# Optimization experiments

Hardware: AMD Instinct MI355X
Metric: run time of the kernel (lower is better)

Reference implementation:

```python
import jax, jax.numpy as jnp
import numpy as np

SIGMA = 1.0
MU = 1.0
STRIKE = 3.0
N_STEPS = 256
BATCH = 131072


def setup_inputs() -> dict:
    key = jax.random.key(0)
    ks = jax.random.split(key, 4)

    def lin(k, o, i):
        # equinox Linear-style uniform init in [-1/sqrt(i), 1/sqrt(i)]
        lim = 1.0 / np.sqrt(i)
        return jax.random.uniform(k, (o, i), jnp.float32, -lim, lim)

    return {
        "noise": jax.random.normal(ks[0], (N_STEPS, BATCH), jnp.float32),
        "ts": jnp.linspace(0.0, 1.0, N_STEPS + 1, dtype=jnp.float32),
        "w": jnp.float32(0.9),  # E[max(S1 - K, 0)] Monte-Carlo constant
        "W1": lin(ks[1], 32, 2), "b1": jnp.zeros((32,), jnp.float32),
        "W2": lin(ks[2], 32, 32), "b2": jnp.zeros((32,), jnp.float32),
        "W3": lin(ks[3], 1, 32), "b3": jnp.zeros((1,), jnp.float32),
    }


def reference(noise, ts, w, W1, b1, W2, b2, W3, b3):
    # Holding strategy MLP: in=[t, s] (2) -> 32 -> 32 -> 1, silu/silu/sigmoid
    def holding(t, s):  # s: [B] -> h: [B]
        x = jnp.stack([jnp.broadcast_to(t, s.shape), s], axis=-1)  # [B,2]
        a = jax.nn.silu(x @ W1.T + b1)
        a = jax.nn.silu(a @ W2.T + b2)
        return jax.nn.sigmoid(a @ W3.T + b3)[:, 0]

    def drift(t, y):  # y: [B,2] -> [B,2]
        s = y[:, 0]
        h = holding(t, s)
        return jnp.stack([MU * s, MU * s * h], axis=-1)

    def diffusion(t, y):  # scalar Brownian noise: diffusion vector [B,2]
        s = y[:, 0]
        h = holding(t, s)
        return jnp.stack([SIGMA * s, SIGMA * s * h], axis=-1)

    dts = jnp.diff(ts)                      # [N]
    dWs = noise * jnp.sqrt(dts)[:, None]    # [N,B] Brownian increments

    def step(y, xs):
        t, dt, dW = xs                      # dW: [B]
        f = drift(t, y)
        g = diffusion(t, y)
        # Milstein correction: directional derivative (Dg . g) via jvp
        _, dg = jax.jvp(lambda yy: diffusion(t, yy), (y,), (g,))
        y1 = (y + f * dt + g * dW[:, None]
              + 0.5 * dg * (dW * dW - dt)[:, None])  # Ito Milstein
        return y1, None

    B = noise.shape[1]
    y0 = jnp.broadcast_to(jnp.array([1.0, 0.0], jnp.float32), (B, 2))
    yT, _ = jax.lax.scan(step, y0, (ts[:-1], dts, dWs))

    s1 = yT[:, 0]
    hedging_pnl = yT[:, 1]
    z = jnp.maximum(0.0, s1 - STRIKE)
    return (z - hedging_pnl - w) ** 2  # [B] per-path loss
```

## Files before the change

### kernel.cpp

```cpp
#include <hip/hip_runtime.h>
#include <hip/hip_fp16.h>
#include <math.h>

#define BATCH 131072
#define NSTEPS 256
#define LGN 7
#define NPTS 128
#define ZSPAN 12.0f
#define ZLO 6.0f
#define ZSCALE (NPTS / ZSPAN)
#define DZ (ZSPAN / NPTS)
#define MU_C 0.72134752044448170367f
#define SD_C 1.4426950408889634f

using f32x2 = __attribute__((ext_vector_type(2))) float;

__device__ __forceinline__ float fast_exp(float x) {
    return __builtin_amdgcn_exp2f(x * 1.44269504088896340736f);
}
__device__ __forceinline__ float fast_rcp(float x) {
    return __builtin_amdgcn_rcpf(x);
}
__device__ __forceinline__ float sigmoidf_fast(float x) {
    return fast_rcp(1.0f + fast_exp(-x));
}

#define REP32(M) M(0) M(1) M(2) M(3) M(4) M(5) M(6) M(7) \
                 M(8) M(9) M(10) M(11) M(12) M(13) M(14) M(15) \
                 M(16) M(17) M(18) M(19) M(20) M(21) M(22) M(23) \
                 M(24) M(25) M(26) M(27) M(28) M(29) M(30) M(31)

#define REP16(M) M(0) M(1) M(2) M(3) M(4) M(5) M(6) M(7) \
                 M(8) M(9) M(10) M(11) M(12) M(13) M(14) M(15)

#define MLP_BODY(W1r, B1, W2r, B2, W3r, b3v, t, s, sd, H, HACC) \
    { \
        const float __t = (t), __s = (s), __sd = (sd); \
        f32x2 acc2 = {(b3v), 0.0f}; \
        REP32(MLP_L1) \
        REP32(MLP_ROW) \
        H = sigmoidf_fast(acc2.x); \
        HACC = acc2.y; \
    }

#define MLP_L1(j) f32x2 at##j; { \
    const float2 wv = W1r[j]; \
    const float z  = fmaf(wv.x, __t, fmaf(wv.y, __s, B1[j])); \
    const float zd = wv.y * __sd; \
    const float sg = sigmoidf_fast(z); \
    const float da = sg * (1.0f + z * (1.0f - sg)); \
    at##j = (f32x2){z * sg, da * zd}; }

#define MLP_ROW(j) { \
    const float4 q0 = W2r[(j) * 8 + 0]; \
    const float4 q1 = W2r[(j) * 8 + 1]; \
    const float4 q2 = W2r[(j) * 8 + 2]; \
    const float4 q3 = W2r[(j) * 8 + 3]; \
    const float4 q4 = W2r[(j) * 8 + 4]; \
    const float4 q5 = W2r[(j) * 8 + 5]; \
    const float4 q6 = W2r[(j) * 8 + 6]; \
    const float4 q7 = W2r[(j) * 8 + 7]; \
    f32x2 zza = {B2[j], 0.0f}; \
    f32x2 zzb = {0.0f, 0.0f}; \
    zza += (f32x2){q0.x, q0.x} * at0;  zzb += (f32x2){q0.y, q0.y} * at1; \
    zza += (f32x2){q0.z, q0.z} * at2;  zzb += (f32x2){q0.w, q0.w} * at3; \
    zza += (f32x2){q1.x, q1.x} * at4;  zzb += (f32x2){q1.y, q1.y} * at5; \
    zza += (f32x2){q1.z, q1.z} * at6;  zzb += (f32x2){q1.w, q1.w} * at7; \
    zza += (f32x2){q2.x, q2.x} * at8;  zzb += (f32x2){q2.y, q2.y} * at9; \
    zza += (f32x2){q2.z, q2.z} * at10; zzb += (f32x2){q2.w, q2.w} * at11; \
    zza += (f32x2){q3.x, q3.x} * at12; zzb += (f32x2){q3.y, q3.y} * at13; \
    zza += (f32x2){q3.z, q3.z} * at14; zzb += (f32x2){q3.w, q3.w} * at15; \
    zza += (f32x2){q4.x, q4.x} * at16; zzb += (f32x2){q4.y, q4.y} * at17; \
    zza += (f32x2){q4.z, q4.z} * at18; zzb += (f32x2){q4.w, q4.w} * at19; \
    zza += (f32x2){q5.x, q5.x} * at20; zzb += (f32x2){q5.y, q5.y} * at21; \
    zza += (f32x2){q5.z, q5.z} * at22; zzb += (f32x2){q5.w, q5.w} * at23; \
    zza += (f32x2){q6.x, q6.x} * at24; zzb += (f32x2){q6.y, q6.y} * at25; \
    zza += (f32x2){q6.z, q6.z} * at26; zzb += (f32x2){q6.w, q6.w} * at27; \
    zza += (f32x2){q7.x, q7.x} * at28; zzb += (f32x2){q7.y, q7.y} * at29; \
    zza += (f32x2){q7.z, q7.z} * at30; zzb += (f32x2){q7.w, q7.w} * at31; \
    const f32x2 zzt = zza + zzb; \
    const float zv  = zzt.x; \
    const float sg  = sigmoidf_fast(zv); \
    const float da  = sg * (1.0f + zv * (1.0f - sg)); \
    const float w3  = W3r[j]; \
    acc2 += (f32x2){w3, w3} * (f32x2){zv * sg, da * zzt.y}; \
}

__global__ __launch_bounds__(256) void table_eval_kernel(
    const float* __restrict__ ts,
    const float* __restrict__ W1, const float* __restrict__ b1,
    const float* __restrict__ W2, const float* __restrict__ b2,
    const float* __restrict__ W3, const float* __restrict__ b3,
    unsigned int* __restrict__ W)
{
    __shared__ __align__(16) float sW1[64];
    __shared__ float sb1[32];
    __shared__ __align__(16) float sW2[1024];
    __shared__ float sb2[32];
    __shared__ float sW3[32];
    __shared__ float sb3[1];

    const int tid = threadIdx.x;
    for (int i = tid; i < 1024; i += 256) sW2[i] = W2[i];
    if (tid < 64) sW1[tid] = W1[tid];
    if (tid < 32) { sb1[tid] = b1[tid]; sb2[tid] = b2[tid]; sW3[tid] = W3[tid]; }
    if (tid == 0) sb3[0] = b3[0];
    __syncthreads();

    const float2* W1r = (const float2*)sW1;
    const float*  B1  = sb1;
    const float4* W2r = (const float4*)sW2;
    const float*  B2  = sb2;
    const float*  W3r = sW3;
    const float   b3v = sb3[0];

    const int gid = blockIdx.x * 256 + tid;
    const int st = gid >> LGN;
    const int k  = gid & (NPTS - 1);

    const float t  = ts[st];
    const float mu = MU_C * t;
    const float sd = SD_C * __builtin_sqrtf(t) + 1e-4f;
    const float zz = fmaf((float)k, DZ, -ZLO);
    const float s  = __builtin_amdgcn_exp2f(fmaf(zz, sd, mu));

    float h, hacc;
    MLP_BODY(W1r, B1, W2r, B2, W3r, b3v, t, s, 1.0f, h, hacc)

    const float q = h * (1.0f - h) * hacc * s;
    __half2 p = __floats2half2_rn(h, q);
    const unsigned int pv = *(unsigned int*)&p;

    W[2 * gid] = pv;
    if (k > 0)         W[2 * gid - 1] = pv;
    if (k == NPTS - 1) W[2 * gid + 1] = pv;
}

__global__ __launch_bounds__(256, 1) void path_kernel(
    const float* __restrict__ noise,
    const float* __restrict__ ts,
    const float* __restrict__ wq,
    const uint2* __restrict__ T2,
    float* __restrict__ out)
{
    __shared__ float4 sdt4[NSTEPS];
    __shared__ float  scr[NSTEPS];
    const int tid = threadIdx.x;
    if (tid < NSTEPS) {
        const float t0  = ts[tid];
        const float dtv = ts[tid + 1] - t0;
        const float sdv = SD_C * __builtin_sqrtf(t0) + 1e-4f;
        const float wp  = fast_rcp(sdv) * ZSCALE;
        const float cp  = ZLO * ZSCALE - MU_C * t0 * wp;
        sdt4[tid] = make_float4(dtv, __builtin_sqrtf(dtv), cp, wp);
        scr[tid]  = 0.69314718056f * fast_rcp(wp);
    }
    __syncthreads();

    const int gid = blockIdx.x * 256 + tid;
    const float* np_ = noise + gid;
    const float umax = (float)NPTS - 1.001f;

    float s   = 1.0f;
    float pnl = 0.0f;

    #define NL0(k) float nA##k = np_[(size_t)(k) * BATCH]; \
                   float nB##k = np_[(size_t)(16 + k) * BATCH];
    REP16(NL0)
    #undef NL0

    #define CHK(k, G, NPv, BASE) \
        const float4 dq##G##k = sdt4[(BASE) + k]; \
        const float dW##G##k  = NPv##k * dq##G##k.y; \
        const float mil##G##k = 0.5f * fmaf(dW##G##k, dW##G##k, -dq##G##k.x); \
        const float Af##G##k  = dq##G##k.x + dW##G##k + mil##G##k; \
        const float sv##G##k  = s; \
        s = fmaf(s, Af##G##k, s); \
        const float P##G##k = sv##G##k * Af##G##k; \
        const float Q##G##k = sv##G##k * mil##G##k; \
        const float x##G##k = __builtin_amdgcn_logf(sv##G##k); \
        const float u##G##k = \
            fminf(fmaxf(fmaf(x##G##k, dq##G##k.w, dq##G##k.z), 0.0f), umax); \
        const int   i0##G##k = (int)u##G##k; \
        const float f##G##k  = u##G##k - (float)i0##G##k; \
        unsigned long long E##G##k = \
            ((const unsigned long long*)(T2 + ((size_t)((BASE) + k) << LGN)))[i0##G##k];

    #define NPF(k, NPv, PFB) NPv##k = np_[(size_t)((PFB) + k) * BATCH];

    #define PNK(k, G, BASE) { \
        const uint2 eu = __builtin_bit_cast(uint2, E##G##k); \
        const float2 a0 = __half22float2(*(const __half2*)&eu.x); \
        const float2 a1 = __half22float2(*(const __half2*)&eu.y); \
        const float cr = scr[(BASE) + k]; \
        const float uu = f##G##k; \
        const float m  = uu * uu; \
        const float n  = m * uu; \
        const float dh = a1.x - a0.x; \
        const float ba = fmaf(-2.0f, n, 3.0f * m);             \
        const float bb = fmaf(-2.0f, m, uu) + n;               \
        const float bc = n - m;                                \
        const float hh = fmaf(dh, ba, a0.x) + cr * fmaf(a0.y, bb, a1.y * bc); \
        const float qq = fmaf(uu, a1.y - a0.y, a0.y); \
        pnl = fmaf(hh, P##G##k, fmaf(qq, Q##G##k, pnl)); }

    #define CHA(k) CHK(k, A, nA, baseA)
    #define CHB(k) CHK(k, B, nB, baseB)
    #define NPA(k) NPF(k, nA, pfA)
    #define NPB(k) NPF(k, nB, pfB)
    #define PNA(k) PNK(k, A, baseA)
    #define PNB(k) PNK(k, B, baseB)

    #pragma unroll 1
    for (int cc = 0; cc < NSTEPS / 32; ++cc) {
        const int baseA = cc * 32;
        const int baseB = cc * 32 + 16;
        const int pfA = min(baseA + 32, NSTEPS - 16);
        const int pfB = min(baseB + 32, NSTEPS - 16);

        REP16(CHA)
        REP16(CHB)
        __builtin_amdgcn_sched_barrier(0);
        REP16(NPA)
        REP16(NPB)
        asm volatile("" : "+v"(EA0), "+v"(EA1), "+v"(EA2),  "+v"(EA3),
                          "+v"(EA4), "+v"(EA5), "+v"(EA6),  "+v"(EA7));
        asm volatile("" : "+v"(EA8), "+v"(EA9), "+v"(EA10), "+v"(EA11),
                          "+v"(EA12),"+v"(EA13),"+v"(EA14), "+v"(EA15));
        asm volatile("" : "+v"(EB0), "+v"(EB1), "+v"(EB2),  "+v"(EB3),
                          "+v"(EB4), "+v"(EB5), "+v"(EB6),  "+v"(EB7));
        asm volatile("" : "+v"(EB8), "+v"(EB9), "+v"(EB10), "+v"(EB11),
                          "+v"(EB12),"+v"(EB13),"+v"(EB14), "+v"(EB15));
        __builtin_amdgcn_sched_barrier(0);
        REP16(PNA)
        REP16(PNB)
    }

    #undef CHA
    #undef CHB
    #undef NPA
    #undef NPB
    #undef PNA
    #undef PNB
    #undef PNK
    #undef NPF
    #undef CHK

    const float z = fmaxf(0.0f, s - 3.0f);
    const float d = z - pnl - wq[0];
    out[gid] = d * d;
}

__global__ __launch_bounds__(256, 3) void deep_hedging_direct(
    const float* __restrict__ noise, const float* __restrict__ ts,
    const float* __restrict__ w,
    const float* __restrict__ W1, const float* __restrict__ b1,
    const float* __restrict__ W2, const float* __restrict__ b2,
    const float* __restrict__ W3, const float* __restrict__ b3,
    float* __restrict__ out)
{
    __shared__ __align__(16) float sW1[64];
    __shared__ float sb1[32];
    __shared__ __align__(16) float sW2[1024];
    __shared__ float sb2[32];
    __shared__ float sW3[32];
    __shared__ float sb3w[2];
    __shared__ float sts[NSTEPS + 1];

    const int tid = threadIdx.x;
    for (int i = tid; i < 1024; i += 256) sW2[i] = W2[i];
    if (tid < 64) sW1[tid] = W1[tid];
    if (tid < 32) { sb1[tid] = b1[tid]; sb2[tid] = b2[tid]; sW3[tid] = W3[tid]; }
    if (tid == 0) { sb3w[0] = b3[0]; sb3w[1] = w[0]; }
    for (int i = tid; i < NSTEPS + 1; i += 256) sts[i] = ts[i];
    __syncthreads();

    const int gid = blockIdx.x * 256 + tid;
    const float* np_ = noise + gid;

    float s   = 1.0f;
    float pnl = 0.0f;
    const float b3v = sb3w[0];
    const float wv_ = sb3w[1];

    #pragma unroll 1
    for (int st = 0; st < NSTEPS; ++st) {
        int zr = 0;
        asm volatile("" : "+v"(zr));
        const float2* W1r = (const float2*)sW1 + zr;
        const float*  B1  = sb1 + zr;
        const float4* W2r = (const float4*)sW2 + zr;
        const float*  B2  = sb2 + zr;
        const float*  W3r = sW3 + zr;

        const float t  = sts[st];
        const float dt = sts[st + 1] - t;
        const float dW = np_[(size_t)st * BATCH] * __builtin_sqrtf(dt);
        const float sd = s;

        float h, hacc;
        MLP_BODY(W1r, B1, W2r, B2, W3r, b3v, t, s, sd, h, hacc)
        const float hd = h * (1.0f - h) * hacc;

        const float mil = 0.5f * (dW * dW - dt);
        const float g1  = s * h;
        const float dg1 = fmaf(sd, h, s * hd);
        const float snew = s + s * dt + s * dW + sd * mil;
        pnl = pnl + g1 * dt + g1 * dW + dg1 * mil;
        s = snew;
    }

    const float z = fmaxf(0.0f, s - 3.0f);
    const float d = z - pnl - wv_;
    out[gid] = d * d;
}

extern "C" void kernel_launch(void* const* d_in, const int* in_sizes, int n_in,
                              void* d_out, int out_size, void* d_ws, size_t ws_size,
                              hipStream_t stream) {
    const float* noise = (const float*)d_in[0];
    const float* ts    = (const float*)d_in[1];
    const float* w     = (const float*)d_in[2];
    const float* W1    = (const float*)d_in[3];
    const float* b1    = (const float*)d_in[4];
    const float* W2    = (const float*)d_in[5];
    const float* b2    = (const float*)d_in[6];
    const float* W3    = (const float*)d_in[7];
    const float* b3    = (const float*)d_in[8];
    float* out = (float*)d_out;

    const size_t nA   = (size_t)NSTEPS * NPTS;
    const size_t need = nA * sizeof(uint2);

    if (ws_size >= need) {
        uint2* T2 = (uint2*)d_ws;

        dim3 tb(256), tg(nA / 256);
        table_eval_kernel<<<tg, tb, 0, stream>>>(ts, W1, b1, W2, b2, W3, b3,
                                                 (unsigned int*)T2);
        dim3 pb(256), pg(BATCH / 256);
        path_kernel<<<pg, pb, 0, stream>>>(noise, ts, w, T2, out);
    } else {
        dim3 grid(BATCH / 256), block(256);
        deep_hedging_direct<<<grid, block, 0, stream>>>(noise, ts, w, W1, b1,
                                                        W2, b2, W3, b3, out);
    }
}
```

Measured before the change: 61.77 us.

## Stage per-chunk lookup table in double-buffered LDS instead of global gathers

The 32-step slice of the precomputed hedge table is now copied cooperatively into a padded, double-buffered shared-memory array each chunk. Per-path interpolation gathers read from LDS rather than issuing scattered global loads. The next slice is prefetched during the current chunk's compute, with a block barrier per chunk. The old scheduling barriers and register pinning are dropped, and launch bounds now allow two blocks per CU, trading extra LDS use and synchronisation for cheaper gathers.

```diff
diff --git a/kernel.cpp b/kernel.cpp
--- a/kernel.cpp
+++ b/kernel.cpp
@@ -12,6 +12,7 @@
 #define DZ (ZSPAN / NPTS)
 #define MU_C 0.72134752044448170367f
 #define SD_C 1.4426950408889634f
+#define LSTRIDE 132
 
 using f32x2 = __attribute__((ext_vector_type(2))) float;
 
@@ -32,6 +33,8 @@
 
 #define REP16(M) M(0) M(1) M(2) M(3) M(4) M(5) M(6) M(7) \
                  M(8) M(9) M(10) M(11) M(12) M(13) M(14) M(15)
+
+#define REP8(M) M(0) M(1) M(2) M(3) M(4) M(5) M(6) M(7)
 
 #define MLP_BODY(W1r, B1, W2r, B2, W3r, b3v, t, s, sd, H, HACC) \
     { \
@@ -136,7 +139,7 @@
     if (k == NPTS - 1) W[2 * gid + 1] = pv;
 }
 
-__global__ __launch_bounds__(256, 1) void path_kernel(
+__global__ __launch_bounds__(256, 2) void path_kernel(
     const float* __restrict__ noise,
     const float* __restrict__ ts,
     const float* __restrict__ wq,
@@ -145,6 +148,8 @@
 {
     __shared__ float4 sdt4[NSTEPS];
     __shared__ float  scr[NSTEPS];
+    __shared__ __align__(16) uint2 Lw[2][32 * LSTRIDE];
+
     const int tid = threadIdx.x;
     if (tid < NSTEPS) {
         const float t0  = ts[tid];
@@ -155,6 +160,14 @@
         sdt4[tid] = make_float4(dtv, __builtin_sqrtf(dtv), cp, wp);
         scr[tid]  = 0.69314718056f * fast_rcp(wp);
     }
+
+    #pragma unroll
+    for (int j = 0; j < 8; ++j) {
+        const uint4 v = ((const uint4*)T2)[j * 256 + tid];
+        const int fl = (j * 256 + tid) * 2;
+        const int r = fl >> 7, i = fl & 127;
+        *(uint4*)&Lw[0][r * LSTRIDE + i] = v;
+    }
     __syncthreads();
 
     const int gid = blockIdx.x * 256 + tid;
@@ -169,7 +182,12 @@
     REP16(NL0)
     #undef NL0
 
-    #define CHK(k, G, NPv, BASE) \
+    #define GLD(j) const uint4 G##j = srcN[(j) * 256 + tid];
+    #define GST(j) { const int fl = ((j) * 256 + tid) * 2; \
+                     const int r = fl >> 7, i = fl & 127; \
+                     *(uint4*)&Lw[nxt][r * LSTRIDE + i] = G##j; }
+
+    #define CHK(k, G, NPv, BASE, R0) \
         const float4 dq##G##k = sdt4[(BASE) + k]; \
         const float dW##G##k  = NPv##k * dq##G##k.y; \
         const float mil##G##k = 0.5f * fmaf(dW##G##k, dW##G##k, -dq##G##k.x); \
@@ -183,15 +201,13 @@
             fminf(fmaxf(fmaf(x##G##k, dq##G##k.w, dq##G##k.z), 0.0f), umax); \
         const int   i0##G##k = (int)u##G##k; \
         const float f##G##k  = u##G##k - (float)i0##G##k; \
-        unsigned long long E##G##k = \
-            ((const unsigned long long*)(T2 + ((size_t)((BASE) + k) << LGN)))[i0##G##k];
+        const uint2 E##G##k = Lrd[((R0) + k) * LSTRIDE + i0##G##k];
 
     #define NPF(k, NPv, PFB) NPv##k = np_[(size_t)((PFB) + k) * BATCH];
 
     #define PNK(k, G, BASE) { \
-        const uint2 eu = __builtin_bit_cast(uint2, E##G##k); \
-        const float2 a0 = __half22float2(*(const __half2*)&eu.x); \
-        const float2 a1 = __half22float2(*(const __half2*)&eu.y); \
+        const float2 a0 = __half22float2(*(const __half2*)&E##G##k.x); \
+        const float2 a1 = __half22float2(*(const __half2*)&E##G##k.y); \
         const float cr = scr[(BASE) + k]; \
         const float uu = f##G##k; \
         const float m  = uu * uu; \
@@ -204,8 +220,8 @@
         const float qq = fmaf(uu, a1.y - a0.y, a0.y); \
         pnl = fmaf(hh, P##G##k, fmaf(qq, Q##G##k, pnl)); }
 
-    #define CHA(k) CHK(k, A, nA, baseA)
-    #define CHB(k) CHK(k, B, nB, baseB)
+    #define CHA(k) CHK(k, A, nA, baseA, 0)
+    #define CHB(k) CHK(k, B, nB, baseB, 16)
     #define NPA(k) NPF(k, nA, pfA)
     #define NPB(k) NPF(k, nB, pfB)
     #define PNA(k) PNK(k, A, baseA)
@@ -213,27 +229,24 @@
 
     #pragma unroll 1
     for (int cc = 0; cc < NSTEPS / 32; ++cc) {
+        const int cur = cc & 1, nxt = cur ^ 1;
         const int baseA = cc * 32;
-        const int baseB = cc * 32 + 16;
-        const int pfA = min(baseA + 32, NSTEPS - 16);
-        const int pfB = min(baseB + 32, NSTEPS - 16);
-
+        const int baseB = baseA + 16;
+        const int nb = min(cc + 1, NSTEPS / 32 - 1);
+        const uint4* srcN = (const uint4*)(T2 + (size_t)nb * 32 * NPTS);
+        const uint2* Lrd = Lw[cur];
+        const int pfA = min(baseA + 32, NSTEPS - 32);
+        const int pfB = pfA + 16;
+
+        REP8(GLD)
         REP16(CHA)
         REP16(CHB)
-        __builtin_amdgcn_sched_barrier(0);
         REP16(NPA)
         REP16(NPB)
-        asm volatile("" : "+v"(EA0), "+v"(EA1), "+v"(EA2),  "+v"(EA3),
-                          "+v"(EA4), "+v"(EA5), "+v"(EA6),  "+v"(EA7));
-        asm volatile("" : "+v"(EA8), "+v"(EA9), "+v"(EA10), "+v"(EA11),
-                          "+v"(EA12),"+v"(EA13),"+v"(EA14), "+v"(EA15));
-        asm volatile("" : "+v"(EB0), "+v"(EB1), "+v"(EB2),  "+v"(EB3),
-                          "+v"(EB4), "+v"(EB5), "+v"(EB6),  "+v"(EB7));
-        asm volatile("" : "+v"(EB8), "+v"(EB9), "+v"(EB10), "+v"(EB11),
-                          "+v"(EB12),"+v"(EB13),"+v"(EB14), "+v"(EB15));
-        __builtin_amdgcn_sched_barrier(0);
         REP16(PNA)
         REP16(PNB)
+        REP8(GST)
+        __syncthreads();
     }
 
     #undef CHA
@@ -245,6 +258,8 @@
     #undef PNK
     #undef NPF
     #undef CHK
+    #undef GLD
+    #undef GST
 
     const float z = fmaxf(0.0f, s - 3.0f);
     const float d = z - pnl - wq[0];
```

New measurement: 74.74 us. 1.21x slower.
